# Performance work log

Hardware: AMD Instinct MI355X
Metric: run time of the kernel (lower is better)

The kernel has to match this reference:

```python
import jax, jax.numpy as jnp
import numpy as np

N_NODES = 100000
N_EDGES = 1600000
D_FEAT = 64
N_CHANNELS = 64


def setup_inputs() -> dict:
    key = jax.random.key(0)
    k1, k2, k3, k4, k5, k6 = jax.random.split(key, 6)
    features = jax.random.normal(k1, (N_NODES, D_FEAT), dtype=jnp.float32)
    kernel = jax.random.normal(k2, (D_FEAT, N_CHANNELS), dtype=jnp.float32) * (1.0 / np.sqrt(D_FEAT))
    bias = jnp.zeros((N_CHANNELS,), dtype=jnp.float32)
    skip_weight = jax.random.normal(k3, (N_CHANNELS,), dtype=jnp.float32) * 0.1
    adj_rows = jax.random.randint(k4, (N_EDGES,), 0, N_NODES, dtype=jnp.int32)
    adj_cols = jax.random.randint(k5, (N_EDGES,), 0, N_NODES, dtype=jnp.int32)
    # normalized adjacency values (positive, ~1/degree scale)
    adj_vals = jax.random.uniform(k6, (N_EDGES,), dtype=jnp.float32) * (1.0 / 16.0)
    return {
        "features": features,
        "kernel": kernel,
        "bias": bias,
        "skip_weight": skip_weight,
        "adj_vals": adj_vals,
        "adj_rows": adj_rows,
        "adj_cols": adj_cols,
    }


def reference(features, kernel, bias, skip_weight, adj_vals, adj_rows, adj_cols):
    # dense transform: [N, d] @ [d, c] + [c]
    h = jnp.matmul(features, kernel) + bias
    # SpMM with COO adjacency: out[i] = sum_e{row[e]=i} vals[e] * h[col[e]]
    msg = adj_vals[:, None] * h[adj_cols]            # [E, c]
    agg = jax.ops.segment_sum(msg, adj_rows, num_segments=features.shape[0])
    # skip (broadcast add of skip_weight, per original code) + activation
    out = agg + skip_weight
    return jax.nn.selu(out)
```

## Files before the change

### kernel.cpp

```cpp
#include <hip/hip_runtime.h>
#include <math.h>

#define N_NODES   100000
#define N_EDGES   1600000
#define D_FEAT    64
#define N_CH      64

#define SELU_SCALE 1.0507009873554805f
#define SELU_ALPHA 1.6732632423543772f

#define SCAN_TPB   256
#define SCAN_ELEMS 1024
#define SCAN_NB    ((N_NODES + SCAN_ELEMS - 1) / SCAN_ELEMS)

#define G_ROWS_PER_WAVE 16
#define G_ROWS_PER_BLOCK (4 * G_ROWS_PER_WAVE)
#define NB_GEMM  ((N_NODES + G_ROWS_PER_BLOCK - 1) / G_ROWS_PER_BLOCK)
#define NB_SCAT4 ((N_EDGES / 4 + 255) / 256)

__device__ __forceinline__ void gemm_body(
    int gb,
    const float* __restrict__ feat,
    const float* __restrict__ W,
    const float* __restrict__ bias,
    float* __restrict__ h)
{
    int lane = threadIdx.x & 63;
    int wave = threadIdx.x >> 6;

    float Wc[D_FEAT];
    #pragma unroll
    for (int k = 0; k < D_FEAT; ++k) Wc[k] = W[k * N_CH + lane];
    float b = bias[lane];

    int row0 = (gb * 4 + wave) * G_ROWS_PER_WAVE;
    for (int r = 0; r < G_ROWS_PER_WAVE; ++r) {
        int row = row0 + r;
        if (row >= N_NODES) return;
        int row_u = __builtin_amdgcn_readfirstlane(row);
        const float* frow = feat + (size_t)row_u * D_FEAT;
        float a0 = b, a1 = 0.f, a2 = 0.f, a3 = 0.f;
        #pragma unroll
        for (int k = 0; k < D_FEAT; k += 4) {
            a0 = fmaf(frow[k + 0], Wc[k + 0], a0);
            a1 = fmaf(frow[k + 1], Wc[k + 1], a1);
            a2 = fmaf(frow[k + 2], Wc[k + 2], a2);
            a3 = fmaf(frow[k + 3], Wc[k + 3], a3);
        }
        h[row * N_CH + lane] = (a0 + a1) + (a2 + a3);
    }
}

__global__ __launch_bounds__(256) void zero_deg_kernel(int* __restrict__ deg)
{
    int i = blockIdx.x * 256 + threadIdx.x;
    if (i < N_NODES) deg[i] = 0;
}

__global__ __launch_bounds__(256) void degree_rank_kernel(
    const int* __restrict__ rows, int* __restrict__ deg, int* __restrict__ rank)
{
    int i = blockIdx.x * 256 + threadIdx.x;
    if (i < N_EDGES / 4) {
        const int4 r = reinterpret_cast<const int4*>(rows)[i];
        int4 k;
        k.x = atomicAdd(&deg[r.x], 1);
        k.y = atomicAdd(&deg[r.y], 1);
        k.z = atomicAdd(&deg[r.z], 1);
        k.w = atomicAdd(&deg[r.w], 1);
        reinterpret_cast<int4*>(rank)[i] = k;
    }
}

__global__ __launch_bounds__(SCAN_TPB) void scan1_kernel(
    const int* __restrict__ deg, int* __restrict__ row_start,
    int* __restrict__ partials)
{
    __shared__ int lds[SCAN_TPB];
    int t = threadIdx.x;
    int base = blockIdx.x * SCAN_ELEMS + t * 4;
    int v0 = (base + 0 < N_NODES) ? deg[base + 0] : 0;
    int v1 = (base + 1 < N_NODES) ? deg[base + 1] : 0;
    int v2 = (base + 2 < N_NODES) ? deg[base + 2] : 0;
    int v3 = (base + 3 < N_NODES) ? deg[base + 3] : 0;
    int s1 = v0, s2 = v0 + v1, s3 = v0 + v1 + v2, tot = v0 + v1 + v2 + v3;
    lds[t] = tot;
    __syncthreads();
    for (int off = 1; off < SCAN_TPB; off <<= 1) {
        int y = (t >= off) ? lds[t - off] : 0;
        __syncthreads();
        lds[t] += y;
        __syncthreads();
    }
    int texcl = (t > 0) ? lds[t - 1] : 0;
    if (t == SCAN_TPB - 1) partials[blockIdx.x] = lds[SCAN_TPB - 1];
    if (base + 0 < N_NODES) row_start[base + 0] = texcl;
    if (base + 1 < N_NODES) row_start[base + 1] = texcl + s1;
    if (base + 2 < N_NODES) row_start[base + 2] = texcl + s2;
    if (base + 3 < N_NODES) row_start[base + 3] = texcl + s3;
}

__global__ __launch_bounds__(128) void scan2_kernel(int* __restrict__ partials)
{
    __shared__ int lds[128];
    int t = threadIdx.x;
    lds[t] = (t < SCAN_NB) ? partials[t] : 0;
    __syncthreads();
    for (int off = 1; off < 128; off <<= 1) {
        int y = (t >= off) ? lds[t - off] : 0;
        __syncthreads();
        lds[t] += y;
        __syncthreads();
    }
    if (t < SCAN_NB) partials[t] = (t > 0) ? lds[t - 1] : 0;
}

__global__ __launch_bounds__(SCAN_TPB) void scan3_kernel(
    int* __restrict__ row_start, const int* __restrict__ partials)
{
    int t = threadIdx.x;
    int add = partials[blockIdx.x];
    int base = blockIdx.x * SCAN_ELEMS + t * 4;
    #pragma unroll
    for (int j = 0; j < 4; ++j) {
        int idx = base + j;
        if (idx < N_NODES) row_start[idx] += add;
    }
    if (blockIdx.x == 0 && t == 0) row_start[N_NODES] = N_EDGES;
}

__global__ __launch_bounds__(256) void scatter_gemm_kernel(
    const int* __restrict__ rows, const int* __restrict__ rank,
    const int* __restrict__ row_start, int* __restrict__ perm,
    const float* __restrict__ feat, const float* __restrict__ W,
    const float* __restrict__ bias, float* __restrict__ h)
{
    if (blockIdx.x < NB_SCAT4) {
        int i = blockIdx.x * 256 + threadIdx.x;
        if (i < N_EDGES / 4) {
            const int4 r  = reinterpret_cast<const int4*>(rows)[i];
            const int4 rk = reinterpret_cast<const int4*>(rank)[i];
            int e0 = i * 4;
            perm[row_start[r.x] + rk.x] = e0 + 0;
            perm[row_start[r.y] + rk.y] = e0 + 1;
            perm[row_start[r.z] + rk.z] = e0 + 2;
            perm[row_start[r.w] + rk.w] = e0 + 3;
        }
    } else {
        gemm_body(blockIdx.x - NB_SCAT4, feat, W, bias, h);
    }
}

__global__ __launch_bounds__(256) void aggregate_kernel(
    const int*   __restrict__ row_start,
    const int*   __restrict__ perm,
    const int*   __restrict__ cols,
    const float* __restrict__ vals,
    const float* __restrict__ h,
    const float* __restrict__ skip,
    float*       __restrict__ out)
{
    int row  = blockIdx.x * 4 + (threadIdx.x >> 6);
    int lane = threadIdx.x & 63;
    if (row >= N_NODES) return;

    int s = row_start[row];
    int e = row_start[row + 1];

    float a0 = 0.f, a1 = 0.f, a2 = 0.f, a3 = 0.f;
    for (int j = s; j < e; j += 64) {
        int cnt = e - j;
        if (cnt > 64) cnt = 64;
        int   c = 0;
        float v = 0.f;
        if (lane < cnt) {
            int eid = perm[j + lane];
            c = cols[eid];
            v = vals[eid];
        }
        int pc = (cnt + 3) & ~3;
        for (int k = 0; k < pc; k += 4) {
            int   c0 = __shfl(c, k + 0, 64);
            float v0 = __shfl(v, k + 0, 64);
            int   c1 = __shfl(c, k + 1, 64);
            float v1 = __shfl(v, k + 1, 64);
            int   c2 = __shfl(c, k + 2, 64);
            float v2 = __shfl(v, k + 2, 64);
            int   c3 = __shfl(c, k + 3, 64);
            float v3 = __shfl(v, k + 3, 64);
            a0 = fmaf(v0, h[c0 * N_CH + lane], a0);
            a1 = fmaf(v1, h[c1 * N_CH + lane], a1);
            a2 = fmaf(v2, h[c2 * N_CH + lane], a2);
            a3 = fmaf(v3, h[c3 * N_CH + lane], a3);
        }
    }
    float x = (a0 + a1) + (a2 + a3) + skip[lane];
    float neg = SELU_SCALE * SELU_ALPHA * expm1f(x);
    out[row * N_CH + lane] = x > 0.f ? SELU_SCALE * x : neg;
}

__global__ __launch_bounds__(256) void gemm_only_kernel(
    const float* __restrict__ feat, const float* __restrict__ W,
    const float* __restrict__ bias, float* __restrict__ h)
{
    gemm_body(blockIdx.x, feat, W, bias, h);
}

__global__ __launch_bounds__(256) void init_out_kernel(
    float* __restrict__ out, const float* __restrict__ skip)
{
    int idx = blockIdx.x * 256 + threadIdx.x;
    if (idx < N_NODES * N_CH) out[idx] = skip[idx & (N_CH - 1)];
}

__global__ __launch_bounds__(256) void edge_kernel(
    const float* __restrict__ vals, const int* __restrict__ rows,
    const int* __restrict__ cols, const float* __restrict__ h,
    float* __restrict__ out)
{
    int e = blockIdx.x * 4 + (threadIdx.x >> 6);
    int lane = threadIdx.x & 63;
    if (e >= N_EDGES) return;
    int row = rows[e];
    int col = cols[e];
    float v = vals[e];
    atomicAdd(&out[row * N_CH + lane], v * h[col * N_CH + lane]);
}

__global__ __launch_bounds__(256) void selu_kernel(float* __restrict__ out)
{
    int idx = blockIdx.x * 256 + threadIdx.x;
    if (idx >= N_NODES * N_CH) return;
    float x = out[idx];
    float neg = SELU_SCALE * SELU_ALPHA * expm1f(x);
    out[idx] = x > 0.f ? SELU_SCALE * x : neg;
}

static inline size_t align256(size_t x) { return (x + 255) & ~(size_t)255; }

extern "C" void kernel_launch(void* const* d_in, const int* in_sizes, int n_in,
                              void* d_out, int out_size, void* d_ws, size_t ws_size,
                              hipStream_t stream)
{
    const float* features = (const float*)d_in[0];
    const float* W        = (const float*)d_in[1];
    const float* bias     = (const float*)d_in[2];
    const float* skip     = (const float*)d_in[3];
    const float* adj_vals = (const float*)d_in[4];
    const int*   adj_rows = (const int*)d_in[5];
    const int*   adj_cols = (const int*)d_in[6];
    float* out = (float*)d_out;

    char* ws = (char*)d_ws;
    size_t off = 0;
    float* h       = (float*)(ws + off);  off = align256(off + (size_t)N_NODES * N_CH * 4);
    int* row_start = (int*)(ws + off);    off = align256(off + (size_t)(N_NODES + 1) * 4);
    int* deg       = (int*)(ws + off);    off = align256(off + (size_t)N_NODES * 4);
    int* rank      = (int*)(ws + off);    off = align256(off + (size_t)N_EDGES * 4);
    int* perm      = (int*)(ws + off);    off = align256(off + (size_t)N_EDGES * 4);
    int* partials  = (int*)(ws + off);    off = align256(off + 128 * 4);
    size_t need = off;

    if (ws_size >= need) {
        zero_deg_kernel<<<(N_NODES + 255) / 256, 256, 0, stream>>>(deg);
        degree_rank_kernel<<<NB_SCAT4, 256, 0, stream>>>(adj_rows, deg, rank);
        scan1_kernel<<<SCAN_NB, SCAN_TPB, 0, stream>>>(deg, row_start, partials);
        scan2_kernel<<<1, 128, 0, stream>>>(partials);
        scan3_kernel<<<SCAN_NB, SCAN_TPB, 0, stream>>>(row_start, partials);
        scatter_gemm_kernel<<<NB_SCAT4 + NB_GEMM, 256, 0, stream>>>(
            adj_rows, rank, row_start, perm, features, W, bias, h);
        aggregate_kernel<<<(N_NODES + 3) / 4, 256, 0, stream>>>(
            row_start, perm, adj_cols, adj_vals, h, skip, out);
    } else {
        gemm_only_kernel<<<NB_GEMM, 256, 0, stream>>>(features, W, bias, h);
        init_out_kernel<<<(N_NODES * N_CH + 255) / 256, 256, 0, stream>>>(out, skip);
        edge_kernel<<<(N_EDGES + 3) / 4, 256, 0, stream>>>(
            adj_vals, adj_rows, adj_cols, h, out);
        selu_kernel<<<(N_NODES * N_CH + 255) / 256, 256, 0, stream>>>(out);
    }
}
```

Before: 348.4 us.

## Scatter packed (col,val) pairs into CSR order and aggregate two rows per wave

The scatter stage now writes each edge's column index and value as one packed 64-bit word in row-sorted order, replacing the permutation array. The aggregation then reads these contiguous pairs instead of making indirect perm→col/val lookups. Each wave handles two rows at once with interleaved accumulators, which raises memory-level parallelism for the gathers from h. The cost is twice the workspace for the packed array and a scatter stage that reads and writes more bytes.

Result: faster. 312.0 us (-10.4%).

```diff
diff --git a/kernel.cpp b/kernel.cpp
--- a/kernel.cpp
+++ b/kernel.cpp
@@ -129,6 +129,95 @@
     if (blockIdx.x == 0 && t == 0) row_start[N_NODES] = N_EDGES;
 }
 
+__global__ __launch_bounds__(256) void scatter_pack_gemm_kernel(
+    const int* __restrict__ rows, const int* __restrict__ rank,
+    const int* __restrict__ cols, const float* __restrict__ vals,
+    const int* __restrict__ row_start, unsigned long long* __restrict__ pack64,
+    const float* __restrict__ feat, const float* __restrict__ W,
+    const float* __restrict__ bias, float* __restrict__ h)
+{
+    if (blockIdx.x < NB_SCAT4) {
+        int i = blockIdx.x * 256 + threadIdx.x;
+        if (i < N_EDGES / 4) {
+            const int4   r  = reinterpret_cast<const int4*>(rows)[i];
+            const int4   rk = reinterpret_cast<const int4*>(rank)[i];
+            const int4   c  = reinterpret_cast<const int4*>(cols)[i];
+            const float4 v  = reinterpret_cast<const float4*>(vals)[i];
+            unsigned long long p0 =
+                ((unsigned long long)__float_as_uint(v.x) << 32) | (unsigned)c.x;
+            unsigned long long p1 =
+                ((unsigned long long)__float_as_uint(v.y) << 32) | (unsigned)c.y;
+            unsigned long long p2 =
+                ((unsigned long long)__float_as_uint(v.z) << 32) | (unsigned)c.z;
+            unsigned long long p3 =
+                ((unsigned long long)__float_as_uint(v.w) << 32) | (unsigned)c.w;
+            __builtin_nontemporal_store(p0, &pack64[row_start[r.x] + rk.x]);
+            __builtin_nontemporal_store(p1, &pack64[row_start[r.y] + rk.y]);
+            __builtin_nontemporal_store(p2, &pack64[row_start[r.z] + rk.z]);
+            __builtin_nontemporal_store(p3, &pack64[row_start[r.w] + rk.w]);
+        }
+    } else {
+        gemm_body(blockIdx.x - NB_SCAT4, feat, W, bias, h);
+    }
+}
+
+__global__ __launch_bounds__(256) void aggregate_pack_kernel(
+    const int*   __restrict__ row_start,
+    const uint2* __restrict__ pack,
+    const float* __restrict__ h,
+    const float* __restrict__ skip,
+    float*       __restrict__ out)
+{
+    int pair = blockIdx.x * 4 + (threadIdx.x >> 6);
+    int lane = threadIdx.x & 63;
+    int r0 = pair * 2;
+    if (r0 >= N_NODES) return;
+    int r1 = r0 + 1;
+
+    int s0 = row_start[r0], e0 = row_start[r0 + 1];
+    int s1 = row_start[r1], e1 = row_start[r1 + 1];
+    float skp = skip[lane];
+
+    float a0 = 0.f, a1 = 0.f, a2 = 0.f, a3 = 0.f;
+    float b0 = 0.f, b1 = 0.f, b2 = 0.f, b3 = 0.f;
+
+    int j0 = s0, j1 = s1;
+    while (j0 < e0 || j1 < e1) {
+        int cnt0 = e0 - j0; cnt0 = cnt0 < 0 ? 0 : (cnt0 > 64 ? 64 : cnt0);
+        int cnt1 = e1 - j1; cnt1 = cnt1 < 0 ? 0 : (cnt1 > 64 ? 64 : cnt1);
+        uint2 p0 = make_uint2(0u, 0u), p1 = make_uint2(0u, 0u);
+        if (lane < cnt0) p0 = pack[j0 + lane];
+        if (lane < cnt1) p1 = pack[j1 + lane];
+        int pc = cnt0 > cnt1 ? cnt0 : cnt1;
+        pc = (pc + 3) & ~3;
+        for (int k = 0; k < pc; k += 4) {
+            int   c00 = __shfl((int)p0.x, k + 0, 64); float v00 = __shfl(__uint_as_float(p0.y), k + 0, 64);
+            int   c10 = __shfl((int)p1.x, k + 0, 64); float v10 = __shfl(__uint_as_float(p1.y), k + 0, 64);
+            int   c01 = __shfl((int)p0.x, k + 1, 64); float v01 = __shfl(__uint_as_float(p0.y), k + 1, 64);
+            int   c11 = __shfl((int)p1.x, k + 1, 64); float v11 = __shfl(__uint_as_float(p1.y), k + 1, 64);
+            int   c02 = __shfl((int)p0.x, k + 2, 64); float v02 = __shfl(__uint_as_float(p0.y), k + 2, 64);
+            int   c12 = __shfl((int)p1.x, k + 2, 64); float v12 = __shfl(__uint_as_float(p1.y), k + 2, 64);
+            int   c03 = __shfl((int)p0.x, k + 3, 64); float v03 = __shfl(__uint_as_float(p0.y), k + 3, 64);
+            int   c13 = __shfl((int)p1.x, k + 3, 64); float v13 = __shfl(__uint_as_float(p1.y), k + 3, 64);
+            a0 = fmaf(v00, h[c00 * N_CH + lane], a0);
+            b0 = fmaf(v10, h[c10 * N_CH + lane], b0);
+            a1 = fmaf(v01, h[c01 * N_CH + lane], a1);
+            b1 = fmaf(v11, h[c11 * N_CH + lane], b1);
+            a2 = fmaf(v02, h[c02 * N_CH + lane], a2);
+            b2 = fmaf(v12, h[c12 * N_CH + lane], b2);
+            a3 = fmaf(v03, h[c03 * N_CH + lane], a3);
+            b3 = fmaf(v13, h[c13 * N_CH + lane], b3);
+        }
+        j0 += 64; j1 += 64;
+    }
+    float x0 = (a0 + a1) + (a2 + a3) + skp;
+    float x1 = (b0 + b1) + (b2 + b3) + skp;
+    float n0 = SELU_SCALE * SELU_ALPHA * expm1f(x0);
+    float n1 = SELU_SCALE * SELU_ALPHA * expm1f(x1);
+    out[r0 * N_CH + lane] = x0 > 0.f ? SELU_SCALE * x0 : n0;
+    out[r1 * N_CH + lane] = x1 > 0.f ? SELU_SCALE * x1 : n1;
+}
+
 __global__ __launch_bounds__(256) void scatter_gemm_kernel(
     const int* __restrict__ rows, const int* __restrict__ rank,
     const int* __restrict__ row_start, int* __restrict__ perm,
@@ -256,12 +345,26 @@
     float* h       = (float*)(ws + off);  off = align256(off + (size_t)N_NODES * N_CH * 4);
     int* row_start = (int*)(ws + off);    off = align256(off + (size_t)(N_NODES + 1) * 4);
     int* deg       = (int*)(ws + off);    off = align256(off + (size_t)N_NODES * 4);
+    int* partials  = (int*)(ws + off);    off = align256(off + 128 * 4);
     int* rank      = (int*)(ws + off);    off = align256(off + (size_t)N_EDGES * 4);
-    int* perm      = (int*)(ws + off);    off = align256(off + (size_t)N_EDGES * 4);
-    int* partials  = (int*)(ws + off);    off = align256(off + 128 * 4);
-    size_t need = off;
-
-    if (ws_size >= need) {
+    size_t need_perm = off + align256((size_t)N_EDGES * 4);
+    size_t need_pack = off + align256((size_t)N_EDGES * 8);
+    int*   perm = (int*)(ws + off);
+    unsigned long long* pack64 = (unsigned long long*)(ws + off);
+    uint2* pack = (uint2*)(ws + off);
+
+    if (ws_size >= need_pack) {
+        zero_deg_kernel<<<(N_NODES + 255) / 256, 256, 0, stream>>>(deg);
+        degree_rank_kernel<<<NB_SCAT4, 256, 0, stream>>>(adj_rows, deg, rank);
+        scan1_kernel<<<SCAN_NB, SCAN_TPB, 0, stream>>>(deg, row_start, partials);
+        scan2_kernel<<<1, 128, 0, stream>>>(partials);
+        scan3_kernel<<<SCAN_NB, SCAN_TPB, 0, stream>>>(row_start, partials);
+        scatter_pack_gemm_kernel<<<NB_SCAT4 + NB_GEMM, 256, 0, stream>>>(
+            adj_rows, rank, adj_cols, adj_vals, row_start, pack64,
+            features, W, bias, h);
+        aggregate_pack_kernel<<<(N_NODES / 2 + 3) / 4, 256, 0, stream>>>(
+            row_start, pack, h, skip, out);
+    } else if (ws_size >= need_perm) {
         zero_deg_kernel<<<(N_NODES + 255) / 256, 256, 0, stream>>>(deg);
         degree_rank_kernel<<<NB_SCAT4, 256, 0, stream>>>(adj_rows, deg, rank);
         scan1_kernel<<<SCAN_NB, SCAN_TPB, 0, stream>>>(deg, row_start, partials);
```
